# Kernel optimization log

Hardware: AMD Instinct MI355X
Metric: run time of the kernel (lower is better)

## Reference

```python
import jax, jax.numpy as jnp
import numpy as np

B, T, V, NS, L, G, H = 16, 256, 18000, 30, 10, 3, 400


def setup_inputs() -> dict:
    key = jax.random.key(0)
    ks = jax.random.split(key, 12)
    return {
        'encoded_hidden': jax.random.normal(ks[0], (1, B, H), jnp.float32),
        'encoded_outputs': jax.random.normal(ks[1], (B, T, H), jnp.float32),
        'emb_weight': jax.random.normal(ks[2], (V, H), jnp.float32) * 0.02,
        'gru_w_ih': jax.random.normal(ks[3], (3 * H, H), jnp.float32) * 0.05,
        'gru_w_hh': jax.random.normal(ks[4], (3 * H, H), jnp.float32) * 0.05,
        'gru_b_ih': jnp.zeros((3 * H,), jnp.float32),
        'gru_b_hh': jnp.zeros((3 * H,), jnp.float32),
        'w_ratio': jax.random.normal(ks[5], (1, 3 * H), jnp.float32) * 0.05,
        'b_ratio': jnp.zeros((1,), jnp.float32),
        'w_gate': jax.random.normal(ks[6], (G, H), jnp.float32) * 0.05,
        'b_gate': jnp.zeros((G,), jnp.float32),
        'slot_emb': jax.random.normal(ks[7], (2 * NS, H), jnp.float32) * 0.1,
        'encoded_lens': jax.random.randint(ks[8], (B,), T // 2, T + 1, jnp.int32),
        'story': jax.random.randint(ks[9], (B, T), 0, V, jnp.int32),
        'target_batches': jax.random.randint(ks[10], (B, NS, L), 0, V, jnp.int32),
        'domain_idx': 2 * jnp.arange(NS, dtype=jnp.int32),
        'slotname_idx': 2 * jnp.arange(NS, dtype=jnp.int32) + 1,
    }


def _forward(encoded_hidden, encoded_outputs, emb_weight, gru_w_ih, gru_w_hh,
             gru_b_ih, gru_b_hh, w_ratio, b_ratio, w_gate, b_gate, slot_emb,
             encoded_lens, story, target_batches, domain_idx, slotname_idx):
    b, t, h = encoded_outputs.shape
    ns, l = target_batches.shape[1], target_batches.shape[2]
    n = ns * b  # flattened slot-major rows: row = slot*b + batch

    combined = slot_emb[domain_idx] + slot_emb[slotname_idx]          # (NS,H)
    dec_in0 = jnp.repeat(combined, b, axis=0)                          # (N,H)
    h0 = jnp.tile(encoded_hidden[0], (ns, 1))                          # (N,H)
    enc = jnp.tile(encoded_outputs, (ns, 1, 1))                        # (N,T,H)
    story_rep = jnp.tile(story, (ns, 1))                               # (N,T)
    lens_rep = jnp.tile(encoded_lens, ns)                              # (N,)
    mask = jnp.arange(t)[None, :] < lens_rep[:, None]                  # (N,T)
    rows = jnp.arange(n)[:, None]

    # teacher forcing: decoder input at step wi>=1 is emb of target at wi-1
    tgt = jnp.transpose(target_batches, (2, 1, 0)).reshape(l, n)       # (L,N)
    dec_inputs = jnp.concatenate([dec_in0[None], emb_weight[tgt[:-1]]], axis=0)

    def step(hid, x):
        gi = x @ gru_w_ih.T + gru_b_ih
        gh = hid @ gru_w_hh.T + gru_b_hh
        i_r, i_z, i_n = jnp.split(gi, 3, axis=-1)
        h_r, h_z, h_n = jnp.split(gh, 3, axis=-1)
        r = jax.nn.sigmoid(i_r + h_r)
        z = jax.nn.sigmoid(i_z + h_z)
        nn_ = jnp.tanh(i_n + r * h_n)
        h_new = (1.0 - z) * nn_ + z * hid                              # (N,H)
        # attend over encoder outputs
        scores = jnp.einsum('nh,nth->nt', h_new, enc)
        scores = jnp.where(mask, scores, -1e9)
        prob = jax.nn.softmax(scores, axis=1)                          # (N,T)
        context = jnp.einsum('nt,nth->nh', prob, enc)                  # (N,H)
        # vocab distribution
        p_vocab = jax.nn.softmax(h_new @ emb_weight.T, axis=1)         # (N,V)
        # pointer-generator mix
        p_gen_vec = jnp.concatenate([h_new, context, x], axis=-1)      # (N,3H)
        switch = jax.nn.sigmoid(p_gen_vec @ w_ratio.T + b_ratio)       # (N,1)
        p_ctx = jnp.zeros_like(p_vocab).at[rows, story_rep].add(prob)  # scatter-add
        final = (1.0 - switch) * p_ctx + switch * p_vocab              # (N,V)
        return h_new, (final, context)

    _, (finals, contexts) = jax.lax.scan(step, h0, dec_inputs)
    points = finals.reshape(l, ns, b, -1).transpose(1, 2, 0, 3)        # (NS,B,L,V)
    gates = (contexts[0] @ w_gate.T + b_gate).reshape(ns, b, -1)       # (NS,B,G)
    return points, gates


def reference(encoded_hidden, encoded_outputs, emb_weight, gru_w_ih, gru_w_hh,
              gru_b_ih, gru_b_hh, w_ratio, b_ratio, w_gate, b_gate, slot_emb,
              encoded_lens, story, target_batches, domain_idx, slotname_idx):
    return _forward(encoded_hidden, encoded_outputs, emb_weight, gru_w_ih,
                    gru_w_hh, gru_b_ih, gru_b_hh, w_ratio, b_ratio, w_gate,
                    b_gate, slot_emb, encoded_lens, story, target_batches,
                    domain_idx, slotname_idx)
```

## Files before the change

### kernel.cpp

```cpp
#include <hip/hip_runtime.h>
#include <hip/hip_bf16.h>

#define Bq 16
#define Tq 256
#define Vq 18000
#define NSq 30
#define Lq 10
#define Gq 3
#define Hq 400
#define Nq (NSq * Bq)
#define H3q (3 * Hq)
#define NKT 25
#define NGV 564
#define NGW 38
#define NGH 15
#define CHq 9000
#define NPB 288
#define NPB_USED 282
#define NGHB 152

typedef __bf16 bf16;
typedef __bf16 bf16x4 __attribute__((ext_vector_type(4)));
typedef __bf16 bf16x8 __attribute__((ext_vector_type(8)));
typedef float floatx16 __attribute__((ext_vector_type(16)));

__global__ __launch_bounds__(256) void k_f2b4(
    const float* __restrict__ src, bf16* __restrict__ dst, const int n4)
{
    int i = blockIdx.x * 256 + threadIdx.x;
    if (i >= n4) return;
    const float4 v = ((const float4*)src)[i];
    bf16x4 o;
    o[0] = (bf16)v.x; o[1] = (bf16)v.y; o[2] = (bf16)v.z; o[3] = (bf16)v.w;
    ((bf16x4*)dst)[i] = o;
}

__global__ __launch_bounds__(256) void k_packf(
    const float* __restrict__ src, bf16* __restrict__ dst,
    const int ngroups, const int nrows)
{
    const int i = blockIdx.x * 256 + threadIdx.x;
    if (i >= ngroups * NKT * 64) return;
    const int lane = i & 63;
    const int kt = (i >> 6) % NKT;
    const int g = i / (NKT * 64);
    int row = g * 32 + (lane & 31);
    if (row >= nrows) row = nrows - 1;
    const int k0 = kt * 16 + (lane >> 5) * 8;
    const float* s = src + (size_t)row * Hq + k0;
    const float4 a = *(const float4*)s;
    const float4 c = *(const float4*)(s + 4);
    bf16x8 o;
    o[0] = (bf16)a.x; o[1] = (bf16)a.y; o[2] = (bf16)a.z; o[3] = (bf16)a.w;
    o[4] = (bf16)c.x; o[5] = (bf16)c.y; o[6] = (bf16)c.z; o[7] = (bf16)c.w;
    *(bf16x8*)(dst + (size_t)i * 8) = o;
}

__global__ __launch_bounds__(256) void k_xball(
    const float* __restrict__ slot_emb, const int* __restrict__ dom,
    const int* __restrict__ slo, const float* __restrict__ emb,
    const int* __restrict__ tgt, bf16* __restrict__ xbp,
    bf16* __restrict__ xlin)
{
    const int i = blockIdx.x * 256 + threadIdx.x;
    if (i >= Lq * NGH * NKT * 64) return;
    const int lane = i & 63;
    const int kt = (i >> 6) % NKT;
    const int gg = i / (NKT * 64);
    const int g = gg % NGH;
    const int s = gg / NGH;
    const int n = g * 32 + (lane & 31);
    const int slot = n >> 4, b = n & (Bq - 1);
    const int k0 = kt * 16 + (lane >> 5) * 8;
    float v[8];
    if (s == 0) {
        const float* p1 = slot_emb + (size_t)dom[slot] * Hq + k0;
        const float* p2 = slot_emb + (size_t)slo[slot] * Hq + k0;
        #pragma unroll
        for (int j = 0; j < 8; ++j) v[j] = p1[j] + p2[j];
    } else {
        const int tv = tgt[(b * NSq + slot) * Lq + (s - 1)];
        const float* p = emb + (size_t)tv * Hq + k0;
        #pragma unroll
        for (int j = 0; j < 8; ++j) v[j] = p[j];
    }
    bf16x8 o;
    #pragma unroll
    for (int j = 0; j < 8; ++j) o[j] = (bf16)v[j];
    *(bf16x8*)(xbp + (size_t)i * 8) = o;
    *(bf16x8*)(xlin + ((size_t)(s * Nq + n)) * Hq + k0) = o;
}

__global__ __launch_bounds__(256) void k_h0(
    const float* __restrict__ ehid, float* __restrict__ h,
    bf16* __restrict__ hbp)
{
    const int i = blockIdx.x * 256 + threadIdx.x;
    if (i >= NGH * NKT * 64) return;
    const int lane = i & 63;
    const int kt = (i >> 6) % NKT;
    const int g = i / (NKT * 64);
    const int n = g * 32 + (lane & 31);
    const int b = n & (Bq - 1);
    const int k0 = kt * 16 + (lane >> 5) * 8;
    const float* s = ehid + (size_t)b * Hq + k0;
    bf16x8 o;
    #pragma unroll
    for (int j = 0; j < 8; ++j) {
        float v = s[j];
        h[(size_t)n * Hq + k0 + j] = v;
        o[j] = (bf16)v;
    }
    *(bf16x8*)(hbp + (size_t)i * 8) = o;
}

__global__ __launch_bounds__(256) void k_gi_all(
    const bf16* __restrict__ xbp, const bf16* __restrict__ wihp,
    float* __restrict__ gi_all)
{
    const int ct = blockIdx.x;
    const int s = blockIdx.y;
    const int wave = threadIdx.x >> 6, lane = threadIdx.x & 63;
    floatx16 acc[4];
    #pragma unroll
    for (int i = 0; i < 4; ++i)
        #pragma unroll
        for (int r = 0; r < 16; ++r) acc[i][r] = 0.f;
    for (int kt = 0; kt < NKT; ++kt) {
        const bf16x8 w = *(const bf16x8*)(wihp + ((size_t)(ct * NKT + kt) * 64 + lane) * 8);
        #pragma unroll
        for (int i = 0; i < 4; ++i) {
            const int g = wave + 4 * i;
            if (g < NGH) {
                const bf16x8 a = *(const bf16x8*)(xbp +
                    ((size_t)((s * NGH + g) * NKT + kt) * 64 + lane) * 8);
                acc[i] = __builtin_amdgcn_mfma_f32_32x32x16_bf16(a, w, acc[i], 0, 0, 0);
            }
        }
    }
    const int j = ct * 32 + (lane & 31);
    if (j >= H3q) return;
    #pragma unroll
    for (int i = 0; i < 4; ++i) {
        const int g = wave + 4 * i;
        if (g < NGH) {
            const int rbase = g * 32 + 4 * (lane >> 5);
            #pragma unroll
            for (int r = 0; r < 16; ++r) {
                const int rr = rbase + (r & 3) + 8 * (r >> 2);
                gi_all[((size_t)(s * Nq + rr)) * H3q + j] = acc[i][r];
            }
        }
    }
}

__global__ __launch_bounds__(256) void k_gh(
    const bf16* __restrict__ hbp, const bf16* __restrict__ whhp,
    float* __restrict__ gh)
{
    const int ct = blockIdx.x;
    const int wave = threadIdx.x >> 6, lane = threadIdx.x & 63;
    const int g = blockIdx.y * 4 + wave;
    if (g >= NGH) return;
    floatx16 acc;
    #pragma unroll
    for (int r = 0; r < 16; ++r) acc[r] = 0.f;
    for (int kt = 0; kt < NKT; ++kt) {
        const bf16x8 a = *(const bf16x8*)(hbp + ((size_t)(g * NKT + kt) * 64 + lane) * 8);
        const bf16x8 w = *(const bf16x8*)(whhp + ((size_t)(ct * NKT + kt) * 64 + lane) * 8);
        acc = __builtin_amdgcn_mfma_f32_32x32x16_bf16(a, w, acc, 0, 0, 0);
    }
    const int j = ct * 32 + (lane & 31);
    if (j >= H3q) return;
    const int rbase = g * 32 + 4 * (lane >> 5);
    #pragma unroll
    for (int r = 0; r < 16; ++r) {
        const int rr = rbase + (r & 3) + 8 * (r >> 2);
        gh[(size_t)rr * H3q + j] = acc[r];
    }
}

__global__ __launch_bounds__(256) void k_attn(
    const float* __restrict__ gi_all, const float* __restrict__ gh,
    const float* __restrict__ b_ih, const float* __restrict__ b_hh,
    float* __restrict__ h, bf16* __restrict__ hbp,
    const bf16* __restrict__ xlin, const bf16* __restrict__ encb,
    const int* __restrict__ lens, const float* __restrict__ w_ratio,
    const float* __restrict__ b_ratio, const float* __restrict__ w_gate,
    const float* __restrict__ b_gate, float* __restrict__ prob,
    float* __restrict__ swp, float* __restrict__ out_gates, const int step)
{
    const int n = blockIdx.x;
    const int b = n & (Bq - 1);
    const int tid = threadIdx.x;
    __shared__ float s_h[Hq];
    __shared__ float s_c[Hq];
    __shared__ float s_p[Tq];
    __shared__ float s_red[4];

    const float* gin = gi_all + ((size_t)step * Nq + n) * H3q;
    const float* ghn = gh + (size_t)n * H3q;
    for (int k = tid; k < Hq; k += 256) {
        float ir = gin[k]          + b_ih[k];
        float hr = ghn[k]          + b_hh[k];
        float iz = gin[Hq + k]     + b_ih[Hq + k];
        float hz = ghn[Hq + k]     + b_hh[Hq + k];
        float in_ = gin[2*Hq + k]  + b_ih[2*Hq + k];
        float hn_ = ghn[2*Hq + k]  + b_hh[2*Hq + k];
        float r = 1.f / (1.f + __expf(-(ir + hr)));
        float z = 1.f / (1.f + __expf(-(iz + hz)));
        float nn = tanhf(in_ + r * hn_);
        float hp = h[(size_t)n * Hq + k];
        float hv = (1.f - z) * nn + z * hp;
        s_h[k] = hv;
        h[(size_t)n * Hq + k] = hv;
        hbp[((size_t)(((n >> 5) * NKT + (k >> 4)) * 64
                      + ((k >> 3) & 1) * 32 + (n & 31))) * 8 + (k & 7)] = (bf16)hv;
    }
    __syncthreads();

    const int t = tid;
    const bf16* erow = encb + (size_t)(b * Tq + t) * Hq;
    float sc = 0.f;
    #pragma unroll 5
    for (int kc = 0; kc < Hq / 8; ++kc) {
        bf16x8 e = *(const bf16x8*)(erow + kc * 8);
        #pragma unroll
        for (int j = 0; j < 8; ++j) sc += s_h[kc * 8 + j] * (float)e[j];
    }
    const int len = lens[b];
    float score = (t < len) ? sc : -1e9f;

    float mx = score;
    for (int off = 32; off > 0; off >>= 1) mx = fmaxf(mx, __shfl_xor(mx, off, 64));
    if ((tid & 63) == 0) s_red[tid >> 6] = mx;
    __syncthreads();
    mx = fmaxf(fmaxf(s_red[0], s_red[1]), fmaxf(s_red[2], s_red[3]));
    float ev = __expf(score - mx);
    float sm = ev;
    for (int off = 32; off > 0; off >>= 1) sm += __shfl_xor(sm, off, 64);
    __syncthreads();
    if ((tid & 63) == 0) s_red[tid >> 6] = sm;
    __syncthreads();
    sm = s_red[0] + s_red[1] + s_red[2] + s_red[3];
    float p = ev / sm;
    s_p[t] = p;
    prob[n * Tq + t] = p;
    __syncthreads();

    for (int k = tid; k < Hq; k += 256) {
        float c = 0.f;
        const bf16* ecol = encb + (size_t)b * Tq * Hq + k;
        for (int tt = 0; tt < Tq; ++tt) c += s_p[tt] * (float)ecol[(size_t)tt * Hq];
        s_c[k] = c;
    }
    __syncthreads();

    const bf16* xr = xlin + ((size_t)step * Nq + n) * Hq;
    float part2 = 0.f;
    for (int k = tid; k < Hq; k += 256) {
        part2 += w_ratio[k]        * s_h[k]
               + w_ratio[Hq + k]   * s_c[k]
               + w_ratio[2*Hq + k] * (float)xr[k];
    }
    for (int off = 32; off > 0; off >>= 1) part2 += __shfl_xor(part2, off, 64);
    __syncthreads();
    if ((tid & 63) == 0) s_red[tid >> 6] = part2;
    __syncthreads();
    if (tid == 0) {
        float tot = s_red[0] + s_red[1] + s_red[2] + s_red[3] + b_ratio[0];
        swp[n] = 1.f / (1.f + __expf(-tot));
    }

    if (step == 0) {
        for (int gg = 0; gg < Gq; ++gg) {
            float pg = 0.f;
            for (int k = tid; k < Hq; k += 256)
                pg += w_gate[gg * Hq + k] * s_c[k];
            for (int off = 32; off > 0; off >>= 1) pg += __shfl_xor(pg, off, 64);
            __syncthreads();
            if ((tid & 63) == 0) s_red[tid >> 6] = pg;
            __syncthreads();
            if (tid == 0)
                out_gates[n * Gq + gg] =
                    s_red[0] + s_red[1] + s_red[2] + s_red[3] + b_gate[gg];
        }
    }
}

__global__ __launch_bounds__(256, 2) void k_vocab_gh(
    const bf16* __restrict__ hbp, const bf16* __restrict__ embp,
    const bf16* __restrict__ whhp, float* __restrict__ eL,
    float* __restrict__ partial, float* __restrict__ gh)
{
    const int wave = threadIdx.x >> 6, lane = threadIdx.x & 63;

    if (blockIdx.x >= NPB_USED) {
        const int bid2 = blockIdx.x - NPB_USED;
        const int ct = bid2 % NGW;
        const int g = (bid2 / NGW) * 4 + wave;
        if (g >= NGH) return;
        floatx16 acc;
        #pragma unroll
        for (int r = 0; r < 16; ++r) acc[r] = 0.f;
        for (int kt = 0; kt < NKT; ++kt) {
            const bf16x8 a = *(const bf16x8*)(hbp + ((size_t)(g * NKT + kt) * 64 + lane) * 8);
            const bf16x8 w = *(const bf16x8*)(whhp + ((size_t)(ct * NKT + kt) * 64 + lane) * 8);
            acc = __builtin_amdgcn_mfma_f32_32x32x16_bf16(a, w, acc, 0, 0, 0);
        }
        const int j = ct * 32 + (lane & 31);
        if (j >= H3q) return;
        const int rbase = g * 32 + 4 * (lane >> 5);
        #pragma unroll
        for (int r = 0; r < 16; ++r) {
            const int rr = rbase + (r & 3) + 8 * (r >> 2);
            gh[(size_t)rr * H3q + j] = acc[r];
        }
        return;
    }

    const int ct2 = blockIdx.x;
    floatx16 acc0[4], acc1[4];
    #pragma unroll
    for (int i = 0; i < 4; ++i)
        #pragma unroll
        for (int r = 0; r < 16; ++r) { acc0[i][r] = 0.f; acc1[i][r] = 0.f; }

    for (int kt = 0; kt < NKT; ++kt) {
        const bf16x8 w0 = *(const bf16x8*)(embp +
            ((size_t)((2 * ct2) * NKT + kt) * 64 + lane) * 8);
        const bf16x8 w1 = *(const bf16x8*)(embp +
            ((size_t)((2 * ct2 + 1) * NKT + kt) * 64 + lane) * 8);
        #pragma unroll
        for (int i = 0; i < 4; ++i) {
            const int g = wave + 4 * i;
            if (g < NGH) {
                const bf16x8 a = *(const bf16x8*)(hbp +
                    ((size_t)(g * NKT + kt) * 64 + lane) * 8);
                acc0[i] = __builtin_amdgcn_mfma_f32_32x32x16_bf16(a, w0, acc0[i], 0, 0, 0);
                acc1[i] = __builtin_amdgcn_mfma_f32_32x32x16_bf16(a, w1, acc1[i], 0, 0, 0);
            }
        }
    }

    const int mcol = lane & 31, half = lane >> 5;
    const int j0 = ct2 * 64 + mcol, j1 = j0 + 32;
    #pragma unroll
    for (int i = 0; i < 4; ++i) {
        const int g = wave + 4 * i;
        if (g >= NGH) continue;
        const int rbase = g * 32 + 4 * half;
        #pragma unroll
        for (int r = 0; r < 16; ++r) {
            const int rr = rbase + (r & 3) + 8 * (r >> 2);
            const float e0 = (j0 < Vq) ? __expf(acc0[i][r]) : 0.f;
            const float e1 = (j1 < Vq) ? __expf(acc1[i][r]) : 0.f;
            if (j0 < Vq) eL[(size_t)rr * Vq + j0] = e0;
            if (j1 < Vq) eL[(size_t)rr * Vq + j1] = e1;
            float v = e0 + e1;
            v += __shfl_xor(v, 16, 64);
            v += __shfl_xor(v, 8, 64);
            v += __shfl_xor(v, 4, 64);
            v += __shfl_xor(v, 2, 64);
            v += __shfl_xor(v, 1, 64);
            if (mcol == 0) partial[(size_t)rr * NPB + ct2] = v;
        }
    }
}

__global__ __launch_bounds__(512) void k_final(
    const float* __restrict__ eL, const float* __restrict__ prob,
    const float* __restrict__ swp, const float* __restrict__ partial,
    const int* __restrict__ story, float* __restrict__ out, const int step)
{
    __shared__ __align__(16) float s_chunk[CHq];
    __shared__ float s_red[8];
    const int n = blockIdx.x;
    const int b = n & (Bq - 1);
    const int tid = threadIdx.x;

    float ps = 0.f;
    if (tid < NPB_USED) ps = partial[(size_t)n * NPB + tid];
    #pragma unroll
    for (int off = 32; off > 0; off >>= 1) ps += __shfl_xor(ps, off, 64);
    if ((tid & 63) == 0) s_red[tid >> 6] = ps;
    __syncthreads();
    float rs = 0.f;
    #pragma unroll
    for (int i = 0; i < 8; ++i) rs += s_red[i];
    const float swv = swp[n];
    const float scale = swv / rs;
    const float4* e4 = (const float4*)(eL + (size_t)n * Vq);
    float* orow = out + ((size_t)n * Lq + step) * Vq;

    #pragma unroll
    for (int c = 0; c < 2; ++c) {
        const int c0 = c * CHq;
        float4* s4 = (float4*)s_chunk;
        for (int v = tid; v < CHq / 4; v += 512) {
            float4 e = e4[c * (CHq / 4) + v];
            e.x *= scale; e.y *= scale; e.z *= scale; e.w *= scale;
            s4[v] = e;
        }
        __syncthreads();
        if (tid < Tq) {
            const int idx = story[b * Tq + tid];
            if (idx >= c0 && idx < c0 + CHq)
                atomicAdd(&s_chunk[idx - c0], (1.f - swv) * prob[n * Tq + tid]);
        }
        __syncthreads();
        float4* o4 = (float4*)(orow + c0);
        for (int v = tid; v < CHq / 4; v += 512)
            o4[v] = s4[v];
        if (c == 0) __syncthreads();
    }
}

extern "C" void kernel_launch(void* const* d_in, const int* in_sizes, int n_in,
                              void* d_out, int out_size, void* d_ws, size_t ws_size,
                              hipStream_t stream)
{
    const float* ehid    = (const float*)d_in[0];
    const float* enc     = (const float*)d_in[1];
    const float* emb     = (const float*)d_in[2];
    const float* w_ih    = (const float*)d_in[3];
    const float* w_hh    = (const float*)d_in[4];
    const float* b_ih    = (const float*)d_in[5];
    const float* b_hh    = (const float*)d_in[6];
    const float* w_ratio = (const float*)d_in[7];
    const float* b_ratio = (const float*)d_in[8];
    const float* w_gate  = (const float*)d_in[9];
    const float* b_gate  = (const float*)d_in[10];
    const float* slot_emb= (const float*)d_in[11];
    const int*  lens     = (const int*)d_in[12];
    const int*  story    = (const int*)d_in[13];
    const int*  tgt      = (const int*)d_in[14];
    const int*  dom      = (const int*)d_in[15];
    const int*  slo      = (const int*)d_in[16];

    float* out = (float*)d_out;
    float* out_gates = out + (size_t)NSq * Bq * Lq * Vq;

    char* w = (char*)d_ws;
    size_t off = 0;
    auto alloc = [&](size_t bytes) -> void* {
        void* p = (void*)(w + off);
        off += (bytes + 255) & ~(size_t)255;
        return p;
    };
    bf16*  xbp    = (bf16*)alloc((size_t)Lq * Nq * Hq * 2);
    bf16*  xlin   = (bf16*)alloc((size_t)Lq * Nq * Hq * 2);
    bf16*  hbp    = (bf16*)alloc((size_t)Nq * Hq * 2);
    float* h      = (float*)alloc((size_t)Nq * Hq * 4);
    float* gi_all = (float*)alloc((size_t)Lq * Nq * H3q * 4);
    float* gh     = (float*)alloc((size_t)Nq * H3q * 4);
    float* prob   = (float*)alloc((size_t)Nq * Tq * 4);
    float* swp    = (float*)alloc((size_t)Nq * 4);
    float* partial= (float*)alloc((size_t)Nq * NPB * 4);
    float* eL     = (float*)alloc((size_t)Nq * Vq * 4);
    bf16*  embp   = (bf16*)alloc((size_t)NGV * NKT * 64 * 8 * 2);
    bf16*  wihp   = (bf16*)alloc((size_t)NGW * NKT * 64 * 8 * 2);
    bf16*  whhp   = (bf16*)alloc((size_t)NGW * NKT * 64 * 8 * 2);
    bf16*  encb   = (bf16*)alloc((size_t)Bq * Tq * Hq * 2);

    {
        int nf;
        nf = NGV * NKT * 64;
        k_packf<<<dim3((nf + 255) / 256), dim3(256), 0, stream>>>(emb, embp, NGV, Vq);
        nf = NGW * NKT * 64;
        k_packf<<<dim3((nf + 255) / 256), dim3(256), 0, stream>>>(w_ih, wihp, NGW, H3q);
        k_packf<<<dim3((nf + 255) / 256), dim3(256), 0, stream>>>(w_hh, whhp, NGW, H3q);
        const int n4 = (Bq * Tq * Hq) / 4;
        k_f2b4<<<dim3((n4 + 255) / 256), dim3(256), 0, stream>>>(enc, encb, n4);
        nf = Lq * NGH * NKT * 64;
        k_xball<<<dim3((nf + 255) / 256), dim3(256), 0, stream>>>(
            slot_emb, dom, slo, emb, tgt, xbp, xlin);
        nf = NGH * NKT * 64;
        k_h0<<<dim3((nf + 255) / 256), dim3(256), 0, stream>>>(ehid, h, hbp);
        k_gi_all<<<dim3(NGW, Lq), dim3(256), 0, stream>>>(xbp, wihp, gi_all);
        k_gh<<<dim3(NGW, 4), dim3(256), 0, stream>>>(hbp, whhp, gh);
    }

    for (int step = 0; step < Lq; ++step) {
        k_attn<<<dim3(Nq), dim3(256), 0, stream>>>(
            gi_all, gh, b_ih, b_hh, h, hbp, xlin, encb, lens, w_ratio, b_ratio,
            w_gate, b_gate, prob, swp, out_gates, step);
        const int nb = NPB_USED + ((step + 1 < Lq) ? NGHB : 0);
        k_vocab_gh<<<dim3(nb), dim3(256), 0, stream>>>(
            hbp, embp, whhp, eL, partial, gh);
        k_final<<<dim3(Nq), dim3(512), 0, stream>>>(
            eL, prob, swp, partial, story, out, step);
    }
}
```

Before: 1.203 ms.

## Fuse next-step attention with current-step output mixing and store vocab exps as bf16

The attention kernel for step s+1 and the final pointer-generator mix for step s now run in one launch, with prob/switch buffers double-buffered so the two halves do not conflict. This removes one launch per step and lets the two kinds of blocks overlap. Vocab exponentials are stored as bf16 instead of fp32 to halve that intermediate traffic, at some cost in output precision. The final stage writes straight to global memory and applies the copy scatter with global atomics instead of staging through LDS. A transposed bf16 encoder copy gives coalesced loads in the score loop.

```diff
diff --git a/kernel.cpp b/kernel.cpp
--- a/kernel.cpp
+++ b/kernel.cpp
@@ -14,7 +14,6 @@
 #define NGV 564
 #define NGW 38
 #define NGH 15
-#define CHq 9000
 #define NPB 288
 #define NPB_USED 282
 #define NGHB 152
@@ -33,6 +32,20 @@
     bf16x4 o;
     o[0] = (bf16)v.x; o[1] = (bf16)v.y; o[2] = (bf16)v.z; o[3] = (bf16)v.w;
     ((bf16x4*)dst)[i] = o;
+}
+
+__global__ __launch_bounds__(256) void k_enct(
+    const bf16* __restrict__ encb, bf16* __restrict__ encT)
+{
+    const int b = blockIdx.x;
+    const int k0 = blockIdx.y * 32;
+    const int t = threadIdx.x;
+    const bf16* src = encb + ((size_t)(b * Tq + t)) * Hq + k0;
+    #pragma unroll
+    for (int j = 0; j < 32; ++j) {
+        if (k0 + j < Hq)
+            encT[((size_t)b * Hq + k0 + j) * Tq + t] = src[j];
+    }
 }
 
 __global__ __launch_bounds__(256) void k_packf(
@@ -180,25 +193,65 @@
     }
 }
 
-__global__ __launch_bounds__(256) void k_attn(
+__global__ __launch_bounds__(256) void k_fused(
+    const int n_attn, const int step_a, const int step_f,
     const float* __restrict__ gi_all, const float* __restrict__ gh,
     const float* __restrict__ b_ih, const float* __restrict__ b_hh,
     float* __restrict__ h, bf16* __restrict__ hbp,
     const bf16* __restrict__ xlin, const bf16* __restrict__ encb,
-    const int* __restrict__ lens, const float* __restrict__ w_ratio,
-    const float* __restrict__ b_ratio, const float* __restrict__ w_gate,
-    const float* __restrict__ b_gate, float* __restrict__ prob,
-    float* __restrict__ swp, float* __restrict__ out_gates, const int step)
-{
-    const int n = blockIdx.x;
-    const int b = n & (Bq - 1);
-    const int tid = threadIdx.x;
+    const bf16* __restrict__ encT, const int* __restrict__ lens,
+    const float* __restrict__ w_ratio, const float* __restrict__ b_ratio,
+    const float* __restrict__ w_gate, const float* __restrict__ b_gate,
+    float* __restrict__ prob_a, float* __restrict__ swp_a,
+    float* __restrict__ out_gates,
+    const bf16* __restrict__ eLb, const float* __restrict__ prob_f,
+    const float* __restrict__ swp_f, const float* __restrict__ partial,
+    const int* __restrict__ story, float* __restrict__ out)
+{
     __shared__ float s_h[Hq];
     __shared__ float s_c[Hq];
     __shared__ float s_p[Tq];
-    __shared__ float s_red[4];
-
-    const float* gin = gi_all + ((size_t)step * Nq + n) * H3q;
+    __shared__ float s_red[8];
+    const int tid = threadIdx.x;
+
+    if ((int)blockIdx.x >= n_attn) {
+        const int n = blockIdx.x - n_attn;
+        const int b = n & (Bq - 1);
+
+        float ps = 0.f;
+        if (tid < NPB_USED) ps = partial[(size_t)n * NPB + tid];
+        if (tid < NPB_USED - 256) ps += partial[(size_t)n * NPB + 256 + tid];
+        #pragma unroll
+        for (int off = 32; off > 0; off >>= 1) ps += __shfl_xor(ps, off, 64);
+        if ((tid & 63) == 0) s_red[tid >> 6] = ps;
+        __syncthreads();
+        const float rs = s_red[0] + s_red[1] + s_red[2] + s_red[3];
+        const float swv = swp_f[n];
+        const float scale = swv / rs;
+
+        const bf16* er = eLb + (size_t)n * Vq;
+        float* orow = out + ((size_t)n * Lq + step_f) * Vq;
+        for (int i8 = tid; i8 < Vq / 8; i8 += 256) {
+            const bf16x8 e = *(const bf16x8*)(er + i8 * 8);
+            float4 o0, o1;
+            o0.x = (float)e[0] * scale; o0.y = (float)e[1] * scale;
+            o0.z = (float)e[2] * scale; o0.w = (float)e[3] * scale;
+            o1.x = (float)e[4] * scale; o1.y = (float)e[5] * scale;
+            o1.z = (float)e[6] * scale; o1.w = (float)e[7] * scale;
+            ((float4*)orow)[i8 * 2]     = o0;
+            ((float4*)orow)[i8 * 2 + 1] = o1;
+        }
+        __syncthreads();
+        __threadfence_block();
+        const int idx = story[b * Tq + tid];
+        atomicAdd(orow + idx, (1.f - swv) * prob_f[(size_t)n * Tq + tid]);
+        return;
+    }
+
+    const int n = blockIdx.x;
+    const int b = n & (Bq - 1);
+
+    const float* gin = gi_all + ((size_t)step_a * Nq + n) * H3q;
     const float* ghn = gh + (size_t)n * H3q;
     for (int k = tid; k < Hq; k += 256) {
         float ir = gin[k]          + b_ih[k];
@@ -220,14 +273,11 @@
     __syncthreads();
 
     const int t = tid;
-    const bf16* erow = encb + (size_t)(b * Tq + t) * Hq;
+    const bf16* ecT = encT + (size_t)b * Hq * Tq + t;
     float sc = 0.f;
-    #pragma unroll 5
-    for (int kc = 0; kc < Hq / 8; ++kc) {
-        bf16x8 e = *(const bf16x8*)(erow + kc * 8);
-        #pragma unroll
-        for (int j = 0; j < 8; ++j) sc += s_h[kc * 8 + j] * (float)e[j];
-    }
+    #pragma unroll 8
+    for (int k = 0; k < Hq; ++k)
+        sc += s_h[k] * (float)ecT[(size_t)k * Tq];
     const int len = lens[b];
     float score = (t < len) ? sc : -1e9f;
 
@@ -245,7 +295,7 @@
     sm = s_red[0] + s_red[1] + s_red[2] + s_red[3];
     float p = ev / sm;
     s_p[t] = p;
-    prob[n * Tq + t] = p;
+    prob_a[(size_t)n * Tq + t] = p;
     __syncthreads();
 
     for (int k = tid; k < Hq; k += 256) {
@@ -256,7 +306,7 @@
     }
     __syncthreads();
 
-    const bf16* xr = xlin + ((size_t)step * Nq + n) * Hq;
+    const bf16* xr = xlin + ((size_t)step_a * Nq + n) * Hq;
     float part2 = 0.f;
     for (int k = tid; k < Hq; k += 256) {
         part2 += w_ratio[k]        * s_h[k]
@@ -269,10 +319,10 @@
     __syncthreads();
     if (tid == 0) {
         float tot = s_red[0] + s_red[1] + s_red[2] + s_red[3] + b_ratio[0];
-        swp[n] = 1.f / (1.f + __expf(-tot));
-    }
-
-    if (step == 0) {
+        swp_a[n] = 1.f / (1.f + __expf(-tot));
+    }
+
+    if (step_a == 0) {
         for (int gg = 0; gg < Gq; ++gg) {
             float pg = 0.f;
             for (int k = tid; k < Hq; k += 256)
@@ -290,7 +340,7 @@
 
 __global__ __launch_bounds__(256, 2) void k_vocab_gh(
     const bf16* __restrict__ hbp, const bf16* __restrict__ embp,
-    const bf16* __restrict__ whhp, float* __restrict__ eL,
+    const bf16* __restrict__ whhp, bf16* __restrict__ eLb,
     float* __restrict__ partial, float* __restrict__ gh)
 {
     const int wave = threadIdx.x >> 6, lane = threadIdx.x & 63;
@@ -355,8 +405,8 @@
             const int rr = rbase + (r & 3) + 8 * (r >> 2);
             const float e0 = (j0 < Vq) ? __expf(acc0[i][r]) : 0.f;
             const float e1 = (j1 < Vq) ? __expf(acc1[i][r]) : 0.f;
-            if (j0 < Vq) eL[(size_t)rr * Vq + j0] = e0;
-            if (j1 < Vq) eL[(size_t)rr * Vq + j1] = e1;
+            if (j0 < Vq) eLb[(size_t)rr * Vq + j0] = (bf16)e0;
+            if (j1 < Vq) eLb[(size_t)rr * Vq + j1] = (bf16)e1;
             float v = e0 + e1;
             v += __shfl_xor(v, 16, 64);
             v += __shfl_xor(v, 8, 64);
@@ -365,54 +415,6 @@
             v += __shfl_xor(v, 1, 64);
             if (mcol == 0) partial[(size_t)rr * NPB + ct2] = v;
         }
-    }
-}
-
-__global__ __launch_bounds__(512) void k_final(
-    const float* __restrict__ eL, const float* __restrict__ prob,
-    const float* __restrict__ swp, const float* __restrict__ partial,
-    const int* __restrict__ story, float* __restrict__ out, const int step)
-{
-    __shared__ __align__(16) float s_chunk[CHq];
-    __shared__ float s_red[8];
-    const int n = blockIdx.x;
-    const int b = n & (Bq - 1);
-    const int tid = threadIdx.x;
-
-    float ps = 0.f;
-    if (tid < NPB_USED) ps = partial[(size_t)n * NPB + tid];
-    #pragma unroll
-    for (int off = 32; off > 0; off >>= 1) ps += __shfl_xor(ps, off, 64);
-    if ((tid & 63) == 0) s_red[tid >> 6] = ps;
-    __syncthreads();
-    float rs = 0.f;
-    #pragma unroll
-    for (int i = 0; i < 8; ++i) rs += s_red[i];
-    const float swv = swp[n];
-    const float scale = swv / rs;
-    const float4* e4 = (const float4*)(eL + (size_t)n * Vq);
-    float* orow = out + ((size_t)n * Lq + step) * Vq;
-
-    #pragma unroll
-    for (int c = 0; c < 2; ++c) {
-        const int c0 = c * CHq;
-        float4* s4 = (float4*)s_chunk;
-        for (int v = tid; v < CHq / 4; v += 512) {
-            float4 e = e4[c * (CHq / 4) + v];
-            e.x *= scale; e.y *= scale; e.z *= scale; e.w *= scale;
-            s4[v] = e;
-        }
-        __syncthreads();
-        if (tid < Tq) {
-            const int idx = story[b * Tq + tid];
-            if (idx >= c0 && idx < c0 + CHq)
-                atomicAdd(&s_chunk[idx - c0], (1.f - swv) * prob[n * Tq + tid]);
-        }
-        __syncthreads();
-        float4* o4 = (float4*)(orow + c0);
-        for (int v = tid; v < CHq / 4; v += 512)
-            o4[v] = s4[v];
-        if (c == 0) __syncthreads();
     }
 }
 
@@ -454,14 +456,17 @@
     float* h      = (float*)alloc((size_t)Nq * Hq * 4);
     float* gi_all = (float*)alloc((size_t)Lq * Nq * H3q * 4);
     float* gh     = (float*)alloc((size_t)Nq * H3q * 4);
-    float* prob   = (float*)alloc((size_t)Nq * Tq * 4);
-    float* swp    = (float*)alloc((size_t)Nq * 4);
+    float* prob0  = (float*)alloc((size_t)Nq * Tq * 4);
+    float* prob1  = (float*)alloc((size_t)Nq * Tq * 4);
+    float* swp0   = (float*)alloc((size_t)Nq * 4);
+    float* swp1   = (float*)alloc((size_t)Nq * 4);
     float* partial= (float*)alloc((size_t)Nq * NPB * 4);
-    float* eL     = (float*)alloc((size_t)Nq * Vq * 4);
+    bf16*  eLb    = (bf16*)alloc((size_t)Nq * Vq * 2);
     bf16*  embp   = (bf16*)alloc((size_t)NGV * NKT * 64 * 8 * 2);
     bf16*  wihp   = (bf16*)alloc((size_t)NGW * NKT * 64 * 8 * 2);
     bf16*  whhp   = (bf16*)alloc((size_t)NGW * NKT * 64 * 8 * 2);
     bf16*  encb   = (bf16*)alloc((size_t)Bq * Tq * Hq * 2);
+    bf16*  encT   = (bf16*)alloc((size_t)Bq * Hq * Tq * 2);
 
     {
         int nf;
@@ -472,6 +477,7 @@
         k_packf<<<dim3((nf + 255) / 256), dim3(256), 0, stream>>>(w_hh, whhp, NGW, H3q);
         const int n4 = (Bq * Tq * Hq) / 4;
         k_f2b4<<<dim3((n4 + 255) / 256), dim3(256), 0, stream>>>(enc, encb, n4);
+        k_enct<<<dim3(Bq, 13), dim3(256), 0, stream>>>(encb, encT);
         nf = Lq * NGH * NKT * 64;
         k_xball<<<dim3((nf + 255) / 256), dim3(256), 0, stream>>>(
             slot_emb, dom, slo, emb, tgt, xbp, xlin);
@@ -481,14 +487,23 @@
         k_gh<<<dim3(NGW, 4), dim3(256), 0, stream>>>(hbp, whhp, gh);
     }
 
-    for (int step = 0; step < Lq; ++step) {
-        k_attn<<<dim3(Nq), dim3(256), 0, stream>>>(
-            gi_all, gh, b_ih, b_hh, h, hbp, xlin, encb, lens, w_ratio, b_ratio,
-            w_gate, b_gate, prob, swp, out_gates, step);
-        const int nb = NPB_USED + ((step + 1 < Lq) ? NGHB : 0);
+    k_fused<<<dim3(Nq), dim3(256), 0, stream>>>(
+        Nq, 0, 0, gi_all, gh, b_ih, b_hh, h, hbp, xlin, encb, encT, lens,
+        w_ratio, b_ratio, w_gate, b_gate, prob0, swp0, out_gates,
+        eLb, prob1, swp1, partial, story, out);
+
+    for (int s = 0; s < Lq; ++s) {
+        const int nb = NPB_USED + ((s + 1 < Lq) ? NGHB : 0);
         k_vocab_gh<<<dim3(nb), dim3(256), 0, stream>>>(
-            hbp, embp, whhp, eL, partial, gh);
-        k_final<<<dim3(Nq), dim3(512), 0, stream>>>(
-            eL, prob, swp, partial, story, out, step);
-    }
-}
+            hbp, embp, whhp, eLb, partial, gh);
+        const int na = (s + 1 < Lq) ? Nq : 0;
+        float* pa = ((s + 1) & 1) ? prob1 : prob0;
+        float* sa = ((s + 1) & 1) ? swp1 : swp0;
+        const float* pf = (s & 1) ? prob1 : prob0;
+        const float* sf = (s & 1) ? swp1 : swp0;
+        k_fused<<<dim3(na + Nq), dim3(256), 0, stream>>>(
+            na, s + 1, s, gi_all, gh, b_ih, b_hh, h, hbp, xlin, encb, encT,
+            lens, w_ratio, b_ratio, w_gate, b_gate, pa, sa, out_gates,
+            eLb, pf, sf, partial, story, out);
+    }
+}
```

Result: slower. 1.326 ms (+10.3%).
